# Optimization experiments

Measured on AMD Instinct MI355X. Metric: run time of the kernel, lower is better.

Reference implementation:

```python
import jax, jax.numpy as jnp
import numpy as np

N_NODES = 50000
N_EDGES = 800000
D = 128


def gcn_conv(x, src, dst, W, b, num_nodes):
    # PyG GCNConv: h = X W; add self-loops; symmetric deg^-1/2 normalization; scatter-add; + bias
    h = x @ W                                   # [N, F_out]
    ones = jnp.ones(src.shape[0], dtype=h.dtype)
    deg = jax.ops.segment_sum(ones, dst, num_segments=num_nodes)  # in-degree incl. self-loops
    dinv = jax.lax.rsqrt(jnp.maximum(deg, 1.0))  # deg >= 1 because of self-loops
    norm = dinv[src] * dinv[dst]                 # [E+N]
    msg = h[src] * norm[:, None]                 # gather + scale
    out = jax.ops.segment_sum(msg, dst, num_segments=num_nodes)
    return out + b


def setup_inputs() -> dict:
    key = jax.random.key(0)
    ks = jax.random.split(key, 6)
    x = jax.random.normal(ks[0], (N_NODES, D), dtype=jnp.float32)
    edge_index = jax.random.randint(ks[1], (2, N_EDGES), 0, N_NODES, dtype=jnp.int64)
    s = 1.0 / np.sqrt(D)
    W1 = jax.random.normal(ks[2], (D, D), dtype=jnp.float32) * s
    W2 = jax.random.normal(ks[3], (D, D), dtype=jnp.float32) * s
    Wg = jax.random.normal(ks[4], (2 * D, D), dtype=jnp.float32) * (1.0 / np.sqrt(2 * D))
    b1 = jnp.zeros((D,), jnp.float32)
    b2 = jnp.zeros((D,), jnp.float32)
    bg = jnp.zeros((D,), jnp.float32)
    return {"x": x, "edge_index": edge_index, "W1": W1, "b1": b1,
            "W2": W2, "b2": b2, "Wg": Wg, "bg": bg}


def reference(x, edge_index, W1, b1, W2, b2, Wg, bg):
    num_nodes = x.shape[0]
    x0 = jnp.clip(x, -100.0, 100.0)
    loop = jnp.arange(num_nodes, dtype=edge_index.dtype)
    src = jnp.concatenate([edge_index[0], loop])
    dst = jnp.concatenate([edge_index[1], loop])
    h = jax.nn.relu(gcn_conv(x0, src, dst, W1, b1, num_nodes))
    # F.dropout(p=0.3, training=False) -> identity at inference
    h = jax.nn.relu(gcn_conv(h, src, dst, W2, b2, num_nodes))
    h = h + x0  # residual (out_channels == in_channels)
    gate = jax.nn.sigmoid(jnp.concatenate([h, x0], axis=1) @ Wg + bg)
    return h * gate
```

## Files before the change

### kernel.cpp

```cpp
#include <hip/hip_runtime.h>
#include <hip/hip_bf16.h>

using short8 = __attribute__((ext_vector_type(8))) short;
using f32x4  = __attribute__((ext_vector_type(4))) float;

static constexpr int NN = 50000;
static constexpr int NE = 800000;
static constexpr int MPAD = 50048;
static constexpr int NB2 = 256;
static constexpr int BNODE = 196;
static constexpr int CAPB = 4096;
static constexpr int NCHB = 200;
static constexpr int CHB = NE / NCHB;

__device__ __forceinline__ float clip100(float v) { return fminf(fmaxf(v, -100.f), 100.f); }
__device__ __forceinline__ unsigned short f2b(float v) {
    __hip_bfloat16 h = __float2bfloat16(v);
    return *reinterpret_cast<unsigned short*>(&h);
}
__device__ __forceinline__ float blo(unsigned int u) { return __uint_as_float(u << 16); }
__device__ __forceinline__ float bhi(unsigned int u) { return __uint_as_float(u & 0xFFFF0000u); }
__device__ __forceinline__ float b2f(unsigned short u) {
    return __uint_as_float(((unsigned int)u) << 16);
}

__global__ __launch_bounds__(256) void k_bucket(const int* __restrict__ idx,
                                                int2* __restrict__ epair,
                                                int* __restrict__ gcur) {
    __shared__ int ls[CHB], ld[CHB];
    __shared__ int bcnt[NB2], bb[NB2], bofs[NB2];
    const int tid = threadIdx.x;
    const int beg = blockIdx.x * CHB;
    for (int i = tid; i < CHB; i += 256) {
        ls[i] = idx[beg + i];
        ld[i] = idx[NE + beg + i];
    }
    bcnt[tid] = 0;
    __syncthreads();
    for (int i = tid; i < CHB; i += 256) atomicAdd(&bcnt[ld[i] / BNODE], 1);
    __syncthreads();
    bb[tid] = atomicAdd(&gcur[tid], bcnt[tid]);
    bofs[tid] = 0;
    __syncthreads();
    for (int i = tid; i < CHB; i += 256) {
        const int d = ld[i];
        const int p = d / BNODE;
        const int pos = atomicAdd(&bofs[p], 1);
        epair[p * CAPB + bb[p] + pos] = make_int2(ls[i], d);
    }
}

__global__ __launch_bounds__(256) void k_scan256(const int* __restrict__ gcur,
                                                 int* __restrict__ bbase,
                                                 int* __restrict__ rowptr) {
    __shared__ int ls[256];
    const int t = threadIdx.x;
    const int own = gcur[t];
    ls[t] = own;
    __syncthreads();
    for (int off = 1; off < 256; off <<= 1) {
        const int add = (t >= off) ? ls[t - off] : 0;
        __syncthreads();
        ls[t] += add;
        __syncthreads();
    }
    bbase[t] = ls[t] - own;
    if (t == 0) rowptr[NN] = NE;
}

__global__ __launch_bounds__(256) void k_sortfill(const int2* __restrict__ epair,
                                                  const int* __restrict__ gcur,
                                                  const int* __restrict__ bbase,
                                                  int* __restrict__ rowptr,
                                                  float* __restrict__ dinv,
                                                  int* __restrict__ esrc) {
    __shared__ int ls[CAPB], ld[CAPB], srt[CAPB];
    __shared__ int cntL[256], sc[256], cur[256];
    const int t = threadIdx.x;
    const int b = blockIdx.x;
    const int ne = gcur[b];
    const int base = bbase[b];
    const int nb0 = b * BNODE;
    const int nn = min(NN - nb0, BNODE);
    for (int i = t; i < ne; i += 256) {
        const int2 p = epair[b * CAPB + i];
        ls[i] = p.x;
        ld[i] = p.y - nb0;
    }
    cntL[t] = 0;
    __syncthreads();
    for (int i = t; i < ne; i += 256) atomicAdd(&cntL[ld[i]], 1);
    __syncthreads();
    sc[t] = cntL[t];
    __syncthreads();
    for (int off = 1; off < 256; off <<= 1) {
        const int add = (t >= off) ? sc[t - off] : 0;
        __syncthreads();
        sc[t] += add;
        __syncthreads();
    }
    const int excl = sc[t] - cntL[t];
    cur[t] = excl;
    if (t < nn) {
        rowptr[nb0 + t] = base + excl;
        dinv[nb0 + t] = rsqrtf(1.f + (float)cntL[t]);
    }
    __syncthreads();
    for (int i = t; i < ne; i += 256) {
        const int pos = atomicAdd(&cur[ld[i]], 1);
        srt[pos] = ls[i];
    }
    __syncthreads();
    for (int i = t; i < ne; i += 256) esrc[base + i] = srt[i];
}

__global__ __launch_bounds__(256) void k_cvtw(const float* __restrict__ W1,
                                              const float* __restrict__ W2,
                                              const float* __restrict__ Wg,
                                              unsigned short* __restrict__ Wt1,
                                              unsigned short* __restrict__ Wt2,
                                              unsigned short* __restrict__ Wgt,
                                              int* __restrict__ gcur) {
    const int i = blockIdx.x * 256 + threadIdx.x;
    if (i < NB2) gcur[i] = 0;
    if (i < 16384) {
        const int n = i >> 7, k = i & 127;
        Wt1[i] = f2b(W1[k * 128 + n]);
    } else if (i < 32768) {
        const int j = i - 16384;
        const int n = j >> 7, k = j & 127;
        Wt2[j] = f2b(W2[k * 128 + n]);
    } else {
        const int j = i - 32768;
        const int n = j >> 8, k = j & 255;
        Wgt[j] = f2b(Wg[k * 128 + n]);
    }
}

template <bool AB16>
__global__ __launch_bounds__(256) void k_mfma_lds(const unsigned short* __restrict__ Ab,
                                                  const float* __restrict__ Af,
                                                  const unsigned short* __restrict__ Wt,
                                                  unsigned short* __restrict__ Cb,
                                                  const float* __restrict__ dinv) {
    __shared__ unsigned short wl[128 * 136];
    const int tid = threadIdx.x;
#pragma unroll
    for (int j = tid; j < 2048; j += 256) {
        const int row = j >> 4, c8 = j & 15;
        *(short8*)(wl + row * 136 + c8 * 8) = *(const short8*)(Wt + row * 128 + c8 * 8);
    }
    __syncthreads();

    const int wv = tid >> 6;
    const int ln = tid & 63;
    const int l16 = ln & 15;
    const int qd = ln >> 4;
    const int rowb = blockIdx.x * 64 + wv * 16;
    const long arow = rowb + l16;
    const int kq = qd * 8;

    f32x4 acc[8];
#pragma unroll
    for (int i = 0; i < 8; ++i) acc[i] = (f32x4){0.f, 0.f, 0.f, 0.f};

#pragma unroll
    for (int kc = 0; kc < 4; ++kc) {
        short8 a;
        if (AB16) {
            a = *(const short8*)(Ab + arow * 128 + kc * 32 + kq);
        } else {
            a = (short8){0, 0, 0, 0, 0, 0, 0, 0};
            if (arow < NN) {
                const float* fp = Af + arow * 128 + kc * 32 + kq;
                const float4 f0 = *(const float4*)fp;
                const float4 f1 = *(const float4*)(fp + 4);
                a[0] = (short)f2b(clip100(f0.x));
                a[1] = (short)f2b(clip100(f0.y));
                a[2] = (short)f2b(clip100(f0.z));
                a[3] = (short)f2b(clip100(f0.w));
                a[4] = (short)f2b(clip100(f1.x));
                a[5] = (short)f2b(clip100(f1.y));
                a[6] = (short)f2b(clip100(f1.z));
                a[7] = (short)f2b(clip100(f1.w));
            }
        }
#pragma unroll
        for (int nt = 0; nt < 8; ++nt) {
            const short8 b = *(const short8*)(wl + (nt * 16 + l16) * 136 + kc * 32 + kq);
            acc[nt] = __builtin_amdgcn_mfma_f32_16x16x32_bf16(a, b, acc[nt], 0, 0, 0);
        }
    }

    const int r0 = rowb + qd * 4;
#pragma unroll
    for (int r = 0; r < 4; ++r) {
        const int row = r0 + r;
        if (row < NN) {
            const float dv = dinv[row];
#pragma unroll
            for (int nt = 0; nt < 8; ++nt) {
                Cb[(long)row * 128 + nt * 16 + l16] = f2b(acc[nt][r] * dv);
            }
        }
    }
}

__global__ __launch_bounds__(256) void k_mfma_gate(const unsigned short* __restrict__ Ab,
                                                   const float* __restrict__ Af,
                                                   const unsigned short* __restrict__ Wt,
                                                   const float* __restrict__ bg,
                                                   float* __restrict__ out) {
    __shared__ unsigned short wl[128 * 264];
    const int tid = threadIdx.x;
#pragma unroll
    for (int j = tid; j < 4096; j += 256) {
        const int row = j >> 5, c8 = j & 31;
        *(short8*)(wl + row * 264 + c8 * 8) = *(const short8*)(Wt + row * 256 + c8 * 8);
    }
    __syncthreads();

    const int wv = tid >> 6;
    const int ln = tid & 63;
    const int l16 = ln & 15;
    const int qd = ln >> 4;
    const int rowb = blockIdx.x * 64 + wv * 16;
    const long arow = rowb + l16;
    const int kq = qd * 8;

    f32x4 acc[8];
#pragma unroll
    for (int i = 0; i < 8; ++i) acc[i] = (f32x4){0.f, 0.f, 0.f, 0.f};

    {
        const unsigned short* ap = Ab + arow * 128 + kq;
#pragma unroll
        for (int kc = 0; kc < 4; ++kc) {
            const short8 a = *(const short8*)(ap + kc * 32);
#pragma unroll
            for (int nt = 0; nt < 8; ++nt) {
                const short8 b = *(const short8*)(wl + (nt * 16 + l16) * 264 + kc * 32 + kq);
                acc[nt] = __builtin_amdgcn_mfma_f32_16x16x32_bf16(a, b, acc[nt], 0, 0, 0);
            }
        }
    }
    {
        const bool valid = arow < NN;
        const float* fp = Af + arow * 128 + kq;
#pragma unroll
        for (int kc = 0; kc < 4; ++kc) {
            short8 a = (short8){0, 0, 0, 0, 0, 0, 0, 0};
            if (valid) {
                const float4 f0 = *(const float4*)(fp + kc * 32);
                const float4 f1 = *(const float4*)(fp + kc * 32 + 4);
                a[0] = (short)f2b(clip100(f0.x));
                a[1] = (short)f2b(clip100(f0.y));
                a[2] = (short)f2b(clip100(f0.z));
                a[3] = (short)f2b(clip100(f0.w));
                a[4] = (short)f2b(clip100(f1.x));
                a[5] = (short)f2b(clip100(f1.y));
                a[6] = (short)f2b(clip100(f1.z));
                a[7] = (short)f2b(clip100(f1.w));
            }
#pragma unroll
            for (int nt = 0; nt < 8; ++nt) {
                const short8 b = *(const short8*)(wl + (nt * 16 + l16) * 264 + 128 + kc * 32 + kq);
                acc[nt] = __builtin_amdgcn_mfma_f32_16x16x32_bf16(a, b, acc[nt], 0, 0, 0);
            }
        }
    }

    const int r0 = rowb + qd * 4;
#pragma unroll
    for (int nt = 0; nt < 8; ++nt) {
        const int col = nt * 16 + l16;
        const float bgv = bg[col];
#pragma unroll
        for (int r = 0; r < 4; ++r) {
            const int row = r0 + r;
            if (row < NN) {
                const float g = 1.f / (1.f + __expf(-(acc[nt][r] + bgv)));
                out[(long)row * 128 + col] = b2f(Ab[(long)row * 128 + col]) * g;
            }
        }
    }
}

template <bool RES>
__global__ __launch_bounds__(256) void k_aggr(const unsigned int* __restrict__ As2,
                                              unsigned short* __restrict__ Bb,
                                              const int* __restrict__ rowptr,
                                              const int* __restrict__ esrc,
                                              const float* __restrict__ dinv,
                                              const float* __restrict__ bias,
                                              const float* __restrict__ x) {
    const int d = (blockIdx.x * 256 + threadIdx.x) >> 6;
    if (d >= NN) return;
    const int lane = threadIdx.x & 63;
    const float dd = dinv[d];

    const unsigned int u = As2[(long)d * 64 + lane];
    float2 acc;
    acc.x = blo(u);
    acc.y = bhi(u);

    const int beg = rowptr[d];
    const int end = rowptr[d + 1];
    int i = beg;
    for (; i + 8 <= end; i += 8) {
        const int s0 = esrc[i + 0], s1 = esrc[i + 1], s2 = esrc[i + 2], s3 = esrc[i + 3];
        const int s4 = esrc[i + 4], s5 = esrc[i + 5], s6 = esrc[i + 6], s7 = esrc[i + 7];
        const unsigned int v0 = As2[(long)s0 * 64 + lane];
        const unsigned int v1 = As2[(long)s1 * 64 + lane];
        const unsigned int v2 = As2[(long)s2 * 64 + lane];
        const unsigned int v3 = As2[(long)s3 * 64 + lane];
        const unsigned int v4 = As2[(long)s4 * 64 + lane];
        const unsigned int v5 = As2[(long)s5 * 64 + lane];
        const unsigned int v6 = As2[(long)s6 * 64 + lane];
        const unsigned int v7 = As2[(long)s7 * 64 + lane];
        acc.x += ((blo(v0) + blo(v1)) + (blo(v2) + blo(v3))) +
                 ((blo(v4) + blo(v5)) + (blo(v6) + blo(v7)));
        acc.y += ((bhi(v0) + bhi(v1)) + (bhi(v2) + bhi(v3))) +
                 ((bhi(v4) + bhi(v5)) + (bhi(v6) + bhi(v7)));
    }
    if (i + 4 <= end) {
        const int s0 = esrc[i + 0], s1 = esrc[i + 1], s2 = esrc[i + 2], s3 = esrc[i + 3];
        const unsigned int v0 = As2[(long)s0 * 64 + lane];
        const unsigned int v1 = As2[(long)s1 * 64 + lane];
        const unsigned int v2 = As2[(long)s2 * 64 + lane];
        const unsigned int v3 = As2[(long)s3 * 64 + lane];
        acc.x += (blo(v0) + blo(v1)) + (blo(v2) + blo(v3));
        acc.y += (bhi(v0) + bhi(v1)) + (bhi(v2) + bhi(v3));
        i += 4;
    }
    for (; i < end; ++i) {
        const unsigned int v = As2[(long)esrc[i] * 64 + lane];
        acc.x += blo(v);
        acc.y += bhi(v);
    }

    const float2 bv = ((const float2*)bias)[lane];
    acc.x = fmaxf(fmaf(acc.x, dd, bv.x), 0.f);
    acc.y = fmaxf(fmaf(acc.y, dd, bv.y), 0.f);
    if (RES) {
        const float2 xv = ((const float2*)x)[(long)d * 64 + lane];
        acc.x += clip100(xv.x);
        acc.y += clip100(xv.y);
    }
    const unsigned int pack = (unsigned int)f2b(acc.x) | ((unsigned int)f2b(acc.y) << 16);
    ((unsigned int*)Bb)[(long)d * 64 + lane] = pack;
}

extern "C" void kernel_launch(void* const* d_in, const int* in_sizes, int n_in,
                              void* d_out, int out_size, void* d_ws, size_t ws_size,
                              hipStream_t stream) {
    const float* x  = (const float*)d_in[0];
    const int*  eix = (const int*)d_in[1];
    const float* W1 = (const float*)d_in[2];
    const float* b1 = (const float*)d_in[3];
    const float* W2 = (const float*)d_in[4];
    const float* b2 = (const float*)d_in[5];
    const float* Wg = (const float*)d_in[6];
    const float* bg = (const float*)d_in[7];
    float* out = (float*)d_out;

    char* ws = (char*)d_ws;
    unsigned short* As   = (unsigned short*)ws;
    unsigned short* hb   = (unsigned short*)(ws + 12812288);
    unsigned short* Wt1  = (unsigned short*)(ws + 25624576);
    unsigned short* Wt2  = (unsigned short*)(ws + 25657344);
    unsigned short* Wgt  = (unsigned short*)(ws + 25690112);
    int*   rowptr = (int*)(ws + 25755648);
    float* dinv   = (float*)(ws + 25956352);
    int*   gcur   = (int*)(ws + 26157056);
    int*   bbase  = (int*)(ws + 26158080);
    int*   esrc   = (int*)(ws + 26159104);
    int2*  epair  = (int2*)(ws + 29359104);

    const int ggrid = MPAD / 64;
    dim3 blk(256);

    k_cvtw<<<256, blk, 0, stream>>>(W1, W2, Wg, Wt1, Wt2, Wgt, gcur);
    k_bucket<<<NCHB, blk, 0, stream>>>(eix, epair, gcur);
    k_scan256<<<1, blk, 0, stream>>>(gcur, bbase, rowptr);
    k_sortfill<<<NB2, blk, 0, stream>>>(epair, gcur, bbase, rowptr, dinv, esrc);

    k_mfma_lds<false><<<ggrid, blk, 0, stream>>>(nullptr, x, Wt1, As, dinv);
    k_aggr<false><<<(NN * 64 + 255) / 256, blk, 0, stream>>>(
        (const unsigned int*)As, hb, rowptr, esrc, dinv, b1, nullptr);

    k_mfma_lds<true><<<ggrid, blk, 0, stream>>>(hb, nullptr, Wt2, As, dinv);
    k_aggr<true><<<(NN * 64 + 255) / 256, blk, 0, stream>>>(
        (const unsigned int*)As, hb, rowptr, esrc, dinv, b2, x);

    k_mfma_gate<<<ggrid, blk, 0, stream>>>(hb, x, Wgt, bg, out);
}
```

Measured before the change: 231.3 us.

## Fold bucket scan into sortfill, halve gate LDS, scalarize aggr node index

Removes the single-block scan kernel launch by having every sortfill block redundantly compute the 256-entry prefix sum over bucket counts in shared memory. The gate GEMM now stages the weight matrix in two halves through a 128x136 LDS buffer instead of a full 128x264 one, cutting shared memory per block to allow more resident blocks, at the cost of extra barriers and reloading. The aggregation kernel marks the destination node index wave-uniform via readfirstlane so index math and loads use scalar registers.

```diff
diff --git a/kernel.cpp b/kernel.cpp
--- a/kernel.cpp
+++ b/kernel.cpp
@@ -50,27 +50,8 @@
     }
 }
 
-__global__ __launch_bounds__(256) void k_scan256(const int* __restrict__ gcur,
-                                                 int* __restrict__ bbase,
-                                                 int* __restrict__ rowptr) {
-    __shared__ int ls[256];
-    const int t = threadIdx.x;
-    const int own = gcur[t];
-    ls[t] = own;
-    __syncthreads();
-    for (int off = 1; off < 256; off <<= 1) {
-        const int add = (t >= off) ? ls[t - off] : 0;
-        __syncthreads();
-        ls[t] += add;
-        __syncthreads();
-    }
-    bbase[t] = ls[t] - own;
-    if (t == 0) rowptr[NN] = NE;
-}
-
 __global__ __launch_bounds__(256) void k_sortfill(const int2* __restrict__ epair,
                                                   const int* __restrict__ gcur,
-                                                  const int* __restrict__ bbase,
                                                   int* __restrict__ rowptr,
                                                   float* __restrict__ dinv,
                                                   int* __restrict__ esrc) {
@@ -78,10 +59,20 @@
     __shared__ int cntL[256], sc[256], cur[256];
     const int t = threadIdx.x;
     const int b = blockIdx.x;
+    sc[t] = gcur[t];
+    __syncthreads();
+    for (int off = 1; off < 256; off <<= 1) {
+        const int add = (t >= off) ? sc[t - off] : 0;
+        __syncthreads();
+        sc[t] += add;
+        __syncthreads();
+    }
     const int ne = gcur[b];
-    const int base = bbase[b];
+    const int base = sc[b] - ne;
     const int nb0 = b * BNODE;
     const int nn = min(NN - nb0, BNODE);
+    if (b == 0 && t == 0) rowptr[NN] = NE;
+
     for (int i = t; i < ne; i += 256) {
         const int2 p = epair[b * CAPB + i];
         ls[i] = p.x;
@@ -211,15 +202,8 @@
                                                    const unsigned short* __restrict__ Wt,
                                                    const float* __restrict__ bg,
                                                    float* __restrict__ out) {
-    __shared__ unsigned short wl[128 * 264];
+    __shared__ unsigned short wl[128 * 136];
     const int tid = threadIdx.x;
-#pragma unroll
-    for (int j = tid; j < 4096; j += 256) {
-        const int row = j >> 5, c8 = j & 31;
-        *(short8*)(wl + row * 264 + c8 * 8) = *(const short8*)(Wt + row * 256 + c8 * 8);
-    }
-    __syncthreads();
-
     const int wv = tid >> 6;
     const int ln = tid & 63;
     const int l16 = ln & 15;
@@ -232,6 +216,12 @@
 #pragma unroll
     for (int i = 0; i < 8; ++i) acc[i] = (f32x4){0.f, 0.f, 0.f, 0.f};
 
+#pragma unroll
+    for (int j = tid; j < 2048; j += 256) {
+        const int row = j >> 4, c8 = j & 15;
+        *(short8*)(wl + row * 136 + c8 * 8) = *(const short8*)(Wt + row * 256 + c8 * 8);
+    }
+    __syncthreads();
     {
         const unsigned short* ap = Ab + arow * 128 + kq;
 #pragma unroll
@@ -239,11 +229,19 @@
             const short8 a = *(const short8*)(ap + kc * 32);
 #pragma unroll
             for (int nt = 0; nt < 8; ++nt) {
-                const short8 b = *(const short8*)(wl + (nt * 16 + l16) * 264 + kc * 32 + kq);
+                const short8 b = *(const short8*)(wl + (nt * 16 + l16) * 136 + kc * 32 + kq);
                 acc[nt] = __builtin_amdgcn_mfma_f32_16x16x32_bf16(a, b, acc[nt], 0, 0, 0);
             }
         }
     }
+    __syncthreads();
+
+#pragma unroll
+    for (int j = tid; j < 2048; j += 256) {
+        const int row = j >> 4, c8 = j & 15;
+        *(short8*)(wl + row * 136 + c8 * 8) = *(const short8*)(Wt + row * 256 + 128 + c8 * 8);
+    }
+    __syncthreads();
     {
         const bool valid = arow < NN;
         const float* fp = Af + arow * 128 + kq;
@@ -264,7 +262,7 @@
             }
 #pragma unroll
             for (int nt = 0; nt < 8; ++nt) {
-                const short8 b = *(const short8*)(wl + (nt * 16 + l16) * 264 + 128 + kc * 32 + kq);
+                const short8 b = *(const short8*)(wl + (nt * 16 + l16) * 136 + kc * 32 + kq);
                 acc[nt] = __builtin_amdgcn_mfma_f32_16x16x32_bf16(a, b, acc[nt], 0, 0, 0);
             }
         }
@@ -294,7 +292,7 @@
                                               const float* __restrict__ dinv,
                                               const float* __restrict__ bias,
                                               const float* __restrict__ x) {
-    const int d = (blockIdx.x * 256 + threadIdx.x) >> 6;
+    const int d = __builtin_amdgcn_readfirstlane((blockIdx.x * 256 + threadIdx.x) >> 6);
     if (d >= NN) return;
     const int lane = threadIdx.x & 63;
     const float dd = dinv[d];
@@ -373,7 +371,6 @@
     int*   rowptr = (int*)(ws + 25755648);
     float* dinv   = (float*)(ws + 25956352);
     int*   gcur   = (int*)(ws + 26157056);
-    int*   bbase  = (int*)(ws + 26158080);
     int*   esrc   = (int*)(ws + 26159104);
     int2*  epair  = (int2*)(ws + 29359104);
 
@@ -382,8 +379,7 @@
 
     k_cvtw<<<256, blk, 0, stream>>>(W1, W2, Wg, Wt1, Wt2, Wgt, gcur);
     k_bucket<<<NCHB, blk, 0, stream>>>(eix, epair, gcur);
-    k_scan256<<<1, blk, 0, stream>>>(gcur, bbase, rowptr);
-    k_sortfill<<<NB2, blk, 0, stream>>>(epair, gcur, bbase, rowptr, dinv, esrc);
+    k_sortfill<<<NB2, blk, 0, stream>>>(epair, gcur, rowptr, dinv, esrc);
 
     k_mfma_lds<false><<<ggrid, blk, 0, stream>>>(nullptr, x, Wt1, As, dinv);
     k_aggr<false><<<(NN * 64 + 255) / 256, blk, 0, stream>>>(
```

Result: faster. 213.8 us (-7.6%).
